# Kernel optimization log

Measured on AMD Instinct MI355X. Metric: run time of the kernel, lower is better.

Reference implementation:

```python
import jax, jax.numpy as jnp
import numpy as np

WS = 16         # window size
NH = 16         # num heads
EPS = 1e-6


def _ln(x):
    m = jnp.mean(x, axis=-1, keepdims=True)
    v = jnp.var(x, axis=-1, keepdims=True)
    return (x - m) * jax.lax.rsqrt(v + EPS)


def _modulate(x, shift, scale):
    return x * (1.0 + scale[:, None, :]) + shift[:, None, :]


def setup_inputs() -> dict:
    key = jax.random.key(0)
    ks = jax.random.split(key, 14)
    D, HD = 1024, 64
    s = 0.02
    return {
        'x': jax.random.normal(ks[0], (4, 4096, D), jnp.float32),
        'c': jax.random.normal(ks[1], (4, D), jnp.float32),
        'qkv_w': jax.random.normal(ks[2], (3 * D, D), jnp.float32) * s,
        'qkv_b': jax.random.normal(ks[3], (3 * D,), jnp.float32) * s,
        'proj_w': jax.random.normal(ks[4], (D, D), jnp.float32) * s,
        'proj_b': jax.random.normal(ks[5], (D,), jnp.float32) * s,
        'rel_pos_h': jax.random.normal(ks[6], (2 * WS - 1, HD), jnp.float32) * s,
        'rel_pos_w': jax.random.normal(ks[7], (2 * WS - 1, HD), jnp.float32) * s,
        'adaLN_w': jax.random.normal(ks[8], (6 * D, D), jnp.float32) * s,
        'adaLN_b': jax.random.normal(ks[9], (6 * D,), jnp.float32) * s,
        'fc1_w': jax.random.normal(ks[10], (4 * D, D), jnp.float32) * s,
        'fc1_b': jax.random.normal(ks[11], (4 * D,), jnp.float32) * s,
        'fc2_w': jax.random.normal(ks[12], (D, 4 * D), jnp.float32) * s,
        'fc2_b': jax.random.normal(ks[13], (D,), jnp.float32) * s,
    }


def _window_attention(x, qkv_w, qkv_b, proj_w, proj_b, rel_pos_h, rel_pos_w):
    # x: [N, T, D] with T = h*w, h = w = sqrt(T)
    N, T, D = x.shape
    h = w = int(round(T ** 0.5))
    nwh, nww = h // WS, w // WS  # grid divides evenly -> no padding
    hd = D // NH
    scale = hd ** -0.5

    # window partition: [N, h, w, D] -> [B, WS, WS, D], B = N*nwh*nww
    xw = x.reshape(N, nwh, WS, nww, WS, D).transpose(0, 1, 3, 2, 4, 5)
    xw = xw.reshape(N * nwh * nww, WS, WS, D)
    B = xw.shape[0]
    L = WS * WS

    qkv = (xw.reshape(B, L, D) @ qkv_w.T + qkv_b)  # [B, L, 3D]
    qkv = qkv.reshape(B, L, 3, NH, hd).transpose(2, 0, 3, 1, 4)  # [3, B, NH, L, hd]
    qkv = qkv.reshape(3, B * NH, L, hd)
    q, k, v = qkv[0], qkv[1], qkv[2]

    attn = jnp.einsum('bqc,bkc->bqk', q * scale, k)  # [B*NH, L, L]

    # decomposed relative position bias (q_size == k_size == WS)
    coords = jnp.arange(WS)
    rel_idx = coords[:, None] - coords[None, :] + (WS - 1)  # [WS, WS]
    Rh = rel_pos_h[rel_idx]  # [WS(q_h), WS(k_h), hd]
    Rw = rel_pos_w[rel_idx]  # [WS(q_w), WS(k_w), hd]
    rq = q.reshape(B * NH, WS, WS, hd)
    rel_h = jnp.einsum('bhwc,hkc->bhwk', rq, Rh)  # [B*NH, WS, WS, WS(kh)]
    rel_w = jnp.einsum('bhwc,wkc->bhwk', rq, Rw)  # [B*NH, WS, WS, WS(kw)]
    attn = (attn.reshape(B * NH, WS, WS, WS, WS)
            + rel_h[:, :, :, :, None]
            + rel_w[:, :, :, None, :]).reshape(B * NH, L, L)

    probs = jax.nn.softmax(attn, axis=-1)
    out = probs @ v  # [B*NH, L, hd]
    out = out.reshape(B, NH, WS, WS, hd).transpose(0, 2, 3, 1, 4).reshape(B, WS, WS, D)
    out = out @ proj_w.T + proj_b

    # window unpartition: [B, WS, WS, D] -> [N, T, D]
    out = out.reshape(N, nwh, nww, WS, WS, D).transpose(0, 1, 3, 2, 4, 5)
    return out.reshape(N, T, D)


def reference(x, c, qkv_w, qkv_b, proj_w, proj_b, rel_pos_h, rel_pos_w,
              adaLN_w, adaLN_b, fc1_w, fc1_b, fc2_w, fc2_b):
    D = x.shape[-1]
    mod = jax.nn.silu(c) @ adaLN_w.T + adaLN_b  # [N, 6D]
    sh_msa, sc_msa, g_msa, sh_mlp, sc_mlp, g_mlp = jnp.split(mod, 6, axis=1)

    a_in = _modulate(_ln(x), sh_msa, sc_msa)
    a_out = _window_attention(a_in, qkv_w, qkv_b, proj_w, proj_b, rel_pos_h, rel_pos_w)
    x = x + g_msa[:, None, :] * a_out

    m_in = _modulate(_ln(x), sh_mlp, sc_mlp)
    hdn = jax.nn.gelu(m_in @ fc1_w.T + fc1_b, approximate=True)
    m_out = hdn @ fc2_w.T + fc2_b
    x = x + g_mlp[:, None, :] * m_out
    return x
```

## Files before the change

### kernel.cpp

```cpp
#include <hip/hip_runtime.h>
#include <cstdint>
#include <cstddef>


typedef float  f32x4    __attribute__((ext_vector_type(4)));
typedef __bf16 bf16x8_t __attribute__((ext_vector_type(8)));
typedef __bf16 bf16x4_t __attribute__((ext_vector_type(4)));

#define DEV __device__ __forceinline__

DEV void gload_lds16(const void* g, void* l) {
    auto gp = (const uint32_t __attribute__((address_space(1)))*)(uintptr_t)g;
    auto lp = (uint32_t __attribute__((address_space(3)))*)(uint32_t)(uintptr_t)l;
    __builtin_amdgcn_global_load_lds(gp, lp, 16, 0, 0);
}

DEV bf16x8_t lds_frag(const __bf16* base, int row, int chunk, int row_elems) {
    return *(const bf16x8_t*)(base + row * row_elems + ((chunk ^ (row & 7)) << 3));
}

DEV bf16x8_t p_frag(const __bf16* base, int row, int chunk) {
    return *(const bf16x8_t*)(base + row * 32 + ((chunk ^ ((row >> 1) & 3)) << 3));
}

DEV int vt_addr(int d, int k) {
    return d * 64 + ((((k >> 3) ^ (d & 7) ^ ((d >> 3) & 7)) << 3) | (k & 7));
}

DEV float gelu_tanh(float v) {
    float u = 0.7978845608028654f * (v + 0.044715f * v * v * v);
    float e = __expf(2.f * u);
    float th = 1.f - 2.f / (e + 1.f);
    return 0.5f * v * (1.f + th);
}

DEV int win2tok(int r) {
    int nb = r >> 12, wi = (r >> 8) & 15, l = r & 255;
    return (nb << 12) + (wi >> 2) * 1024 + (l >> 4) * 64 + (wi & 3) * 16 + (l & 15);
}

__global__ void silu_k(const float* __restrict__ c, float* __restrict__ o, int n) {
    int i = blockIdx.x * 256 + threadIdx.x;
    if (i < n) { float v = c[i]; o[i] = v / (1.f + __expf(-v)); }
}

__global__ void zero_k(float* o, int n) {
    int i = blockIdx.x * 256 + threadIdx.x;
    if (i < n) o[i] = 0.f;
}

__global__ void conv_bf16(const float* __restrict__ s, __bf16* __restrict__ d, int n4) {
    int i = blockIdx.x * 256 + threadIdx.x;
    if (i < n4) {
        float4 v = ((const float4*)s)[i];
        bf16x4_t o; o[0] = (__bf16)v.x; o[1] = (__bf16)v.y; o[2] = (__bf16)v.z; o[3] = (__bf16)v.w;
        ((bf16x4_t*)d)[i] = o;
    }
}

__global__ __launch_bounds__(256)
void mod_gemv(const float* __restrict__ sc, const float* __restrict__ w,
              const float* __restrict__ b, float* __restrict__ mod) {
    int o = (blockIdx.x << 2) + (threadIdx.x >> 6);
    int lane = threadIdx.x & 63;
    int n = o / 6144, col = o % 6144;
    const float4* wr = (const float4*)(w + (size_t)col * 1024);
    const float4* sr = (const float4*)(sc + n * 1024);
    float acc = 0.f;
    #pragma unroll 4
    for (int i = lane; i < 256; i += 64) {
        float4 a = wr[i], x = sr[i];
        acc += a.x * x.x + a.y * x.y + a.z * x.z + a.w * x.w;
    }
    #pragma unroll
    for (int m = 1; m < 64; m <<= 1) acc += __shfl_xor(acc, m);
    if (lane == 0) mod[o] = acc + b[col];
}

__global__ __launch_bounds__(256)
void ln_mod_k(const float* __restrict__ src, const float* __restrict__ mod,
              int sh_off, int sc_off, __bf16* __restrict__ out, int permute, int r0) {
    int rl = blockIdx.x;
    int r = rl + r0;
    int nb = r >> 12;
    int t = permute ? win2tok(r) : r;
    float4 v = ((const float4*)(src + (size_t)t * 1024))[threadIdx.x];
    float s  = v.x + v.y + v.z + v.w;
    float sq = v.x * v.x + v.y * v.y + v.z * v.z + v.w * v.w;
    #pragma unroll
    for (int m = 1; m < 64; m <<= 1) { s += __shfl_xor(s, m); sq += __shfl_xor(sq, m); }
    __shared__ float ps[4], pq[4];
    int wv = threadIdx.x >> 6, ln = threadIdx.x & 63;
    if (ln == 0) { ps[wv] = s; pq[wv] = sq; }
    __syncthreads();
    s  = ps[0] + ps[1] + ps[2] + ps[3];
    sq = pq[0] + pq[1] + pq[2] + pq[3];
    float mean = s * (1.f / 1024.f);
    float var  = sq * (1.f / 1024.f) - mean * mean;
    float rstd = rsqrtf(var + 1e-6f);
    int c = threadIdx.x << 2;
    const float* mrow = mod + nb * 6144;
    float4 scv = *(const float4*)(mrow + sc_off + c);
    float4 shv = *(const float4*)(mrow + sh_off + c);
    bf16x4_t o;
    o[0] = (__bf16)((v.x - mean) * rstd * (1.f + scv.x) + shv.x);
    o[1] = (__bf16)((v.y - mean) * rstd * (1.f + scv.y) + shv.y);
    o[2] = (__bf16)((v.z - mean) * rstd * (1.f + scv.z) + shv.z);
    o[3] = (__bf16)((v.w - mean) * rstd * (1.f + scv.w) + shv.w);
    *(bf16x4_t*)(out + (size_t)rl * 1024 + c) = o;
}

template <int PM, int PN>
DEV void mfma16(f32x4 (&acc)[8][4], bf16x8_t (&fa)[4][2], bf16x8_t (&fb)[2][2][2]) {
    #pragma unroll
    for (int ks = 0; ks < 2; ++ks)
        #pragma unroll
        for (int mi = 0; mi < 4; ++mi)
            #pragma unroll
            for (int nn = 0; nn < 2; ++nn)
                acc[PM * 4 + mi][PN * 2 + nn] = __builtin_amdgcn_mfma_f32_16x16x32_bf16(
                    fa[mi][ks], fb[PN][nn][ks], acc[PM * 4 + mi][PN * 2 + nn], 0, 0, 0);
}

template <int EPI>
__global__ __launch_bounds__(512)
void gemm256(const __bf16* __restrict__ A, const __bf16* __restrict__ B,
             const float* __restrict__ bias, void* __restrict__ Cout,
             const float* __restrict__ extra, const float* __restrict__ mod,
             int N, int K, int r0) {
    extern __shared__ __align__(16) char smem[];
    __bf16* lA = (__bf16*)smem;
    __bf16* lB = lA + 2 * 256 * 64;
    const int tid = threadIdx.x, lane = tid & 63, wv = tid >> 6;
    const int wr = wv >> 2, wc = wv & 3;
    const int bm = blockIdx.y << 8, bn = blockIdx.x << 8;

    f32x4 acc[8][4];
    const f32x4 z4 = {0.f, 0.f, 0.f, 0.f};
    #pragma unroll
    for (int i = 0; i < 8; ++i)
        #pragma unroll
        for (int j = 0; j < 4; ++j) acc[i][j] = z4;

    bf16x8_t fa[4][2], fb[2][2][2];
    const int gc8 = (((lane & 7) ^ (lane >> 3)) << 3);

    auto stageA = [&](int buf, int k0, int h) {
        #pragma unroll
        for (int j = 0; j < 2; ++j) {
            int rb = (h << 6) + (j << 7) + (wv << 3);
            gload_lds16(A + (size_t)(bm + rb + (lane >> 3)) * K + k0 + gc8,
                        lA + buf * 16384 + rb * 64);
        }
    };
    auto stageB = [&](int buf, int k0, int h) {
        #pragma unroll
        for (int j = 0; j < 2; ++j) {
            int rb = (h << 5) + (j << 7) + ((wv & 3) << 3) + ((wv >> 2) << 6);
            gload_lds16(B + (size_t)(bn + rb + (lane >> 3)) * K + k0 + gc8,
                        lB + buf * 16384 + rb * 64);
        }
    };
    auto readA = [&](int buf, int pm) {
        #pragma unroll
        for (int mi = 0; mi < 4; ++mi)
            #pragma unroll
            for (int ks = 0; ks < 2; ++ks)
                fa[mi][ks] = lds_frag(lA + buf * 16384,
                                      (wr << 7) + (pm << 6) + (mi << 4) + (lane & 15),
                                      (ks << 2) + (lane >> 4), 64);
    };
    auto readB = [&](int buf, int pn) {
        #pragma unroll
        for (int ni = 0; ni < 2; ++ni)
            #pragma unroll
            for (int ks = 0; ks < 2; ++ks)
                fb[pn][ni][ks] = lds_frag(lB + buf * 16384,
                                          (wc << 6) + (pn << 5) + (ni << 4) + (lane & 15),
                                          (ks << 2) + (lane >> 4), 64);
    };

    const int nt = K >> 6;
    stageA(0, 0, 0); stageB(0, 0, 0); stageB(0, 0, 1); stageA(0, 0, 1);

    int cur = 0;
    for (int t = 0; t < nt - 1; ++t) {
        const int nk0 = (t + 1) << 6;
        stageA(cur ^ 1, nk0, 0);
        asm volatile("s_waitcnt vmcnt(6)" ::: "memory");
        __builtin_amdgcn_s_barrier();
        __builtin_amdgcn_sched_barrier(0);
        readA(cur, 0); readB(cur, 0);
        asm volatile("s_waitcnt lgkmcnt(0)" ::: "memory");
        __builtin_amdgcn_sched_barrier(0);
        __builtin_amdgcn_s_setprio(1); mfma16<0, 0>(acc, fa, fb); __builtin_amdgcn_s_setprio(0);
        stageB(cur ^ 1, nk0, 0);
        asm volatile("s_waitcnt vmcnt(6)" ::: "memory");
        __builtin_amdgcn_s_barrier();
        __builtin_amdgcn_sched_barrier(0);
        readB(cur, 1);
        asm volatile("s_waitcnt lgkmcnt(0)" ::: "memory");
        __builtin_amdgcn_sched_barrier(0);
        __builtin_amdgcn_s_setprio(1); mfma16<0, 1>(acc, fa, fb); __builtin_amdgcn_s_setprio(0);
        stageB(cur ^ 1, nk0, 1);
        asm volatile("s_waitcnt vmcnt(6)" ::: "memory");
        __builtin_amdgcn_s_barrier();
        __builtin_amdgcn_sched_barrier(0);
        readA(cur, 1);
        asm volatile("s_waitcnt lgkmcnt(0)" ::: "memory");
        __builtin_amdgcn_sched_barrier(0);
        __builtin_amdgcn_s_setprio(1); mfma16<1, 0>(acc, fa, fb); __builtin_amdgcn_s_setprio(0);
        stageA(cur ^ 1, nk0, 1);
        __builtin_amdgcn_s_setprio(1); mfma16<1, 1>(acc, fa, fb); __builtin_amdgcn_s_setprio(0);
        cur ^= 1;
    }
    asm volatile("s_waitcnt vmcnt(4)" ::: "memory");
    __builtin_amdgcn_s_barrier();
    __builtin_amdgcn_sched_barrier(0);
    readA(cur, 0); readB(cur, 0);
    asm volatile("s_waitcnt lgkmcnt(0)" ::: "memory");
    __builtin_amdgcn_sched_barrier(0);
    __builtin_amdgcn_s_setprio(1); mfma16<0, 0>(acc, fa, fb); __builtin_amdgcn_s_setprio(0);
    asm volatile("s_waitcnt vmcnt(2)" ::: "memory");
    __builtin_amdgcn_s_barrier();
    __builtin_amdgcn_sched_barrier(0);
    readB(cur, 1);
    asm volatile("s_waitcnt lgkmcnt(0)" ::: "memory");
    __builtin_amdgcn_sched_barrier(0);
    __builtin_amdgcn_s_setprio(1); mfma16<0, 1>(acc, fa, fb); __builtin_amdgcn_s_setprio(0);
    asm volatile("s_waitcnt vmcnt(0)" ::: "memory");
    __builtin_amdgcn_s_barrier();
    __builtin_amdgcn_sched_barrier(0);
    readA(cur, 1);
    asm volatile("s_waitcnt lgkmcnt(0)" ::: "memory");
    __builtin_amdgcn_sched_barrier(0);
    __builtin_amdgcn_s_setprio(1); mfma16<1, 0>(acc, fa, fb); __builtin_amdgcn_s_setprio(0);
    __builtin_amdgcn_s_setprio(1); mfma16<1, 1>(acc, fa, fb); __builtin_amdgcn_s_setprio(0);

    #pragma unroll
    for (int am = 0; am < 8; ++am) {
        #pragma unroll
        for (int j = 0; j < 4; ++j) {
            int m = bm + (wr << 7) + (am << 4) + ((lane >> 4) << 2) + j;
            #pragma unroll
            for (int an = 0; an < 4; ++an) {
                int n = bn + (wc << 6) + (an << 4) + (lane & 15);
                float v = acc[am][an][j] + bias[n];
                if constexpr (EPI == 0) {
                    ((__bf16*)Cout)[(size_t)m * N + n] = (__bf16)v;
                } else if constexpr (EPI == 1) {
                    int mg = m + r0;
                    int tr = win2tok(mg);
                    float g = mod[(mg >> 12) * 6144 + 2048 + n];
                    ((float*)Cout)[(size_t)tr * 1024 + n] = extra[(size_t)tr * 1024 + n] + g * v;
                } else if constexpr (EPI == 2) {
                    ((__bf16*)Cout)[(size_t)m * N + n] = (__bf16)gelu_tanh(v);
                } else {
                    int mg = m + r0;
                    float g = mod[(mg >> 12) * 6144 + 5120 + n];
                    ((float*)Cout)[(size_t)mg * 1024 + n] = extra[(size_t)mg * 1024 + n] + g * v;
                }
            }
        }
    }
}

__global__ __launch_bounds__(256)
void tab_k(const __bf16* __restrict__ qkv, const float* __restrict__ relh,
           const float* __restrict__ relw, __bf16* __restrict__ tab) {
    __shared__ __bf16 lR[2][31][72];
    for (int i = threadIdx.x; i < 1984; i += 256) {
        int row = i >> 6, c = i & 63;
        lR[0][row][c] = (__bf16)relh[i];
        lR[1][row][c] = (__bf16)relw[i];
    }
    __syncthreads();
    const int h = blockIdx.y;
    const int r = threadIdx.x >> 1, half = threadIdx.x & 1;
    const int l = blockIdx.x * 128 + r;
    const int lw = l & 255;
    const int qi = lw >> 4, qj = lw & 15;
    const __bf16* qrow = qkv + (size_t)l * 3072 + h * 64;
    float qq[64];
    #pragma unroll
    for (int c8 = 0; c8 < 8; ++c8) {
        bf16x8_t q8 = *(const bf16x8_t*)(qrow + (c8 << 3));
        #pragma unroll
        for (int e = 0; e < 8; ++e) qq[c8 * 8 + e] = (float)q8[e];
    }
    bf16x8_t oh, ow;
    #pragma unroll
    for (int kk = 0; kk < 8; ++kk) {
        int kg = (half << 3) + kk;
        const __bf16* Rh = &lR[0][qi - kg + 15][0];
        const __bf16* Rw = &lR[1][qj - kg + 15][0];
        float ah = 0.f, aw = 0.f;
        #pragma unroll
        for (int c8 = 0; c8 < 8; ++c8) {
            bf16x8_t r1 = *(const bf16x8_t*)(Rh + (c8 << 3));
            bf16x8_t r2 = *(const bf16x8_t*)(Rw + (c8 << 3));
            #pragma unroll
            for (int e = 0; e < 8; ++e) {
                ah += qq[c8 * 8 + e] * (float)r1[e];
                aw += qq[c8 * 8 + e] * (float)r2[e];
            }
        }
        oh[kk] = (__bf16)ah; ow[kk] = (__bf16)aw;
    }
    size_t idx = ((size_t)(l >> 8) * 16 + h) * 256 + lw;
    *(bf16x8_t*)(tab + idx * 32 + (half << 3))      = oh;
    *(bf16x8_t*)(tab + idx * 32 + 16 + (half << 3)) = ow;
}

__global__ __launch_bounds__(256, 3)
void attn_k(const __bf16* __restrict__ qkv, const __bf16* __restrict__ tab,
            __bf16* __restrict__ out) {
    __shared__ __align__(16) __bf16 lP[4][32 * 32];
    __shared__ __align__(16) __bf16 lKt[2][64 * 64];
    __shared__ __align__(16) __bf16 lVt[2][64 * 64];
    __shared__ __align__(16) __bf16 lTab[128 * 32];

    const int blk = blockIdx.x;
    const int winc = blk >> 5, h = (blk >> 1) & 15, qh = blk & 1;
    const int tid = threadIdx.x, lane = tid & 63, wv = tid >> 6;
    const __bf16* base = qkv + (size_t)winc * 256 * 3072 + h * 64;
    const int q0 = qh << 7;

    {
        const __bf16* ts = tab + (((size_t)winc * 16 + h) * 256 + q0) * 32;
        #pragma unroll
        for (int q = 0; q < 2; ++q) {
            int c = (wv << 1) + q;
            gload_lds16(ts + c * 512 + lane * 8, lTab + c * 512);
        }
    }
    bf16x8_t qf[2][2];
    #pragma unroll
    for (int mi = 0; mi < 2; ++mi)
        #pragma unroll
        for (int ks = 0; ks < 2; ++ks) {
            int l = q0 + (wv << 5) + (mi << 4) + (lane & 15);
            qf[mi][ks] = *(const bf16x8_t*)(base + (size_t)l * 3072 + (((ks << 2) + (lane >> 4)) << 3));
        }
    {
        const __bf16* kb = base + 1024;
        #pragma unroll
        for (int q = 0; q < 2; ++q) {
            int c = (wv << 1) + q;
            int kl = (c << 3) + (lane >> 3);
            gload_lds16(kb + (size_t)kl * 3072 + (((lane & 7) ^ (lane >> 3)) << 3),
                        lKt[0] + c * 512);
        }
        const __bf16* vb = base + 2048;
        bf16x8_t a = *(const bf16x8_t*)(vb + (size_t)(tid >> 3) * 3072 + ((tid & 7) << 3));
        bf16x8_t b = *(const bf16x8_t*)(vb + (size_t)(32 + (tid >> 3)) * 3072 + ((tid & 7) << 3));
        int lc = tid & 7;
        #pragma unroll
        for (int e = 0; e < 8; ++e) {
            lVt[0][vt_addr(lc * 8 + e, tid >> 3)]        = a[e];
            lVt[0][vt_addr(lc * 8 + e, 32 + (tid >> 3))] = b[e];
        }
    }
    __syncthreads();

    float twv[2][4];
    #pragma unroll
    for (int mi = 0; mi < 2; ++mi)
        #pragma unroll
        for (int j = 0; j < 4; ++j) {
            int qr = (wv << 5) + (mi << 4) + ((lane >> 4) << 2) + j;
            twv[mi][j] = (float)lTab[qr * 32 + 16 + (lane & 15)];
        }

    const f32x4 z4 = {0.f, 0.f, 0.f, 0.f};
    f32x4 oacc[2][4];
    #pragma unroll
    for (int a = 0; a < 2; ++a)
        #pragma unroll
        for (int b = 0; b < 4; ++b) oacc[a][b] = z4;
    float rsum[2][4];
    #pragma unroll
    for (int a = 0; a < 2; ++a)
        #pragma unroll
        for (int j = 0; j < 4; ++j) rsum[a][j] = 0.f;
    __bf16* lPw = lP[wv];

    int cur = 0;
    for (int kt = 0; kt < 4; ++kt) {
        const bool pre = (kt < 3);
        bf16x8_t v8a, v8b;
        if (pre) {
            const __bf16* kb = base + 1024 + (size_t)(kt + 1) * 64 * 3072;
            #pragma unroll
            for (int q = 0; q < 2; ++q) {
                int c = (wv << 1) + q;
                int kl = (c << 3) + (lane >> 3);
                gload_lds16(kb + (size_t)kl * 3072 + (((lane & 7) ^ (lane >> 3)) << 3),
                            lKt[cur ^ 1] + c * 512);
            }
            const __bf16* vb = base + 2048 + (size_t)(kt + 1) * 64 * 3072;
            v8a = *(const bf16x8_t*)(vb + (size_t)(tid >> 3) * 3072 + ((tid & 7) << 3));
            v8b = *(const bf16x8_t*)(vb + (size_t)(32 + (tid >> 3)) * 3072 + ((tid & 7) << 3));
        }

        f32x4 s[2][4];
        #pragma unroll
        for (int a = 0; a < 2; ++a)
            #pragma unroll
            for (int b = 0; b < 4; ++b) s[a][b] = z4;
        #pragma unroll
        for (int ks = 0; ks < 2; ++ks) {
            bf16x8_t kf[4];
            #pragma unroll
            for (int ni = 0; ni < 4; ++ni)
                kf[ni] = lds_frag(lKt[cur], (ni << 4) + (lane & 15), (ks << 2) + (lane >> 4), 64);
            #pragma unroll
            for (int mi = 0; mi < 2; ++mi)
                #pragma unroll
                for (int ni = 0; ni < 4; ++ni)
                    s[mi][ni] = __builtin_amdgcn_mfma_f32_16x16x32_bf16(qf[mi][ks], kf[ni], s[mi][ni], 0, 0, 0);
        }

        #pragma unroll
        for (int mi = 0; mi < 2; ++mi) {
            #pragma unroll
            for (int j = 0; j < 4; ++j) {
                int qr = (wv << 5) + (mi << 4) + ((lane >> 4) << 2) + j;
                bf16x4_t th4 = *(const bf16x4_t*)(lTab + qr * 32 + (kt << 2));
                float rs = 0.f;
                #pragma unroll
                for (int ni = 0; ni < 4; ++ni) {
                    float p = __expf(s[mi][ni][j] * 0.125f + (float)th4[ni] + twv[mi][j]);
                    s[mi][ni][j] = p;
                    rs += p;
                }
                rsum[mi][j] += rs;
            }
        }

        #pragma unroll
        for (int hf = 0; hf < 2; ++hf) {
            #pragma unroll
            for (int mi = 0; mi < 2; ++mi) {
                #pragma unroll
                for (int j = 0; j < 4; ++j) {
                    int rl = (mi << 4) + ((lane >> 4) << 2) + j;
                    #pragma unroll
                    for (int b = 0; b < 2; ++b) {
                        int col = (b << 4) + (lane & 15);
                        lPw[rl * 32 + ((((col >> 3) ^ ((rl >> 1) & 3)) << 3) | (col & 7))] =
                            (__bf16)s[mi][(hf << 1) + b][j];
                    }
                }
            }
            bf16x8_t pf[2], vf[4];
            #pragma unroll
            for (int mi = 0; mi < 2; ++mi)
                pf[mi] = p_frag(lPw, (mi << 4) + (lane & 15), lane >> 4);
            #pragma unroll
            for (int no = 0; no < 4; ++no) {
                int d = (no << 4) + (lane & 15);
                vf[no] = *(const bf16x8_t*)(lVt[cur] + vt_addr(d, ((hf << 2) + (lane >> 4)) << 3));
            }
            #pragma unroll
            for (int mi = 0; mi < 2; ++mi)
                #pragma unroll
                for (int no = 0; no < 4; ++no)
                    oacc[mi][no] = __builtin_amdgcn_mfma_f32_16x16x32_bf16(pf[mi], vf[no], oacc[mi][no], 0, 0, 0);
        }

        if (pre) {
            int lc = tid & 7;
            #pragma unroll
            for (int e = 0; e < 8; ++e) {
                lVt[cur ^ 1][vt_addr(lc * 8 + e, tid >> 3)]        = v8a[e];
                lVt[cur ^ 1][vt_addr(lc * 8 + e, 32 + (tid >> 3))] = v8b[e];
            }
        }
        __syncthreads();
        cur ^= 1;
    }

    #pragma unroll
    for (int mi = 0; mi < 2; ++mi) {
        #pragma unroll
        for (int j = 0; j < 4; ++j) {
            float rs = rsum[mi][j];
            #pragma unroll
            for (int msk = 1; msk < 16; msk <<= 1) rs += __shfl_xor(rs, msk);
            float inv = 1.f / rs;
            int l = q0 + (wv << 5) + (mi << 4) + ((lane >> 4) << 2) + j;
            #pragma unroll
            for (int no = 0; no < 4; ++no) {
                int col = (no << 4) + (lane & 15);
                out[(size_t)(winc * 256 + l) * 1024 + h * 64 + col] = (__bf16)(oacc[mi][no][j] * inv);
            }
        }
    }
}

extern "C" void kernel_launch(void* const* d_in, const int* in_sizes, int n_in,
                              void* d_out, int out_size, void* d_ws, size_t ws_size,
                              hipStream_t stream) {
    const float* x      = (const float*)d_in[0];
    const float* c      = (const float*)d_in[1];
    const float* qkv_w  = (const float*)d_in[2];
    const float* qkv_b  = (const float*)d_in[3];
    const float* proj_w = (const float*)d_in[4];
    const float* proj_b = (const float*)d_in[5];
    const float* rel_h  = (const float*)d_in[6];
    const float* rel_w  = (const float*)d_in[7];
    const float* ada_w  = (const float*)d_in[8];
    const float* ada_b  = (const float*)d_in[9];
    const float* fc1_w  = (const float*)d_in[10];
    const float* fc1_b  = (const float*)d_in[11];
    const float* fc2_w  = (const float*)d_in[12];
    const float* fc2_b  = (const float*)d_in[13];
    float* xo = (float*)d_out;

    char* ws = (char*)d_ws;
    const size_t MB = 1ull << 20;
    int CH = 0;
    const int cands[7] = {16384, 8192, 4096, 2048, 1024, 512, 256};
    for (int i = 0; i < 7; ++i)
        if (26 * MB + (size_t)cands[i] * 10240 <= ws_size) { CH = cands[i]; break; }
    if (CH == 0) {
        zero_k<<<65536, 256, 0, stream>>>(xo, 16777216);
        return;
    }
    const int NCH = 16384 / CH;

    const int LDSB = 131072;
    hipFuncSetAttribute((const void*)&gemm256<0>, hipFuncAttributeMaxDynamicSharedMemorySize, LDSB);
    hipFuncSetAttribute((const void*)&gemm256<1>, hipFuncAttributeMaxDynamicSharedMemorySize, LDSB);
    hipFuncSetAttribute((const void*)&gemm256<2>, hipFuncAttributeMaxDynamicSharedMemorySize, LDSB);
    hipFuncSetAttribute((const void*)&gemm256<3>, hipFuncAttributeMaxDynamicSharedMemorySize, LDSB);

    float*  ws_silu = (float*)(ws);
    float*  ws_mod  = (float*)(ws + 65536);
    __bf16* w_qkv   = (__bf16*)(ws + 1 * MB);
    __bf16* w_proj  = (__bf16*)(ws + 7 * MB);
    __bf16* w_fc1   = (__bf16*)(ws + 9 * MB);
    __bf16* w_fc2   = (__bf16*)(ws + 17 * MB);
    __bf16* bufA    = (__bf16*)(ws + 26 * MB);
    __bf16* bufB    = (__bf16*)(ws + 26 * MB + (size_t)CH * 2048);
    __bf16* tabbuf  = bufB + (size_t)CH * 3072;

    silu_k   <<<16,   256, 0, stream>>>(c, ws_silu, 4096);
    mod_gemv <<<6144, 256, 0, stream>>>(ws_silu, ada_w, ada_b, ws_mod);
    conv_bf16<<<3072, 256, 0, stream>>>(qkv_w,  w_qkv,  786432);
    conv_bf16<<<1024, 256, 0, stream>>>(proj_w, w_proj, 262144);
    conv_bf16<<<4096, 256, 0, stream>>>(fc1_w,  w_fc1,  1048576);
    conv_bf16<<<4096, 256, 0, stream>>>(fc2_w,  w_fc2,  1048576);

    for (int ci = 0; ci < NCH; ++ci) {
        int r0 = ci * CH;
        ln_mod_k<<<CH, 256, 0, stream>>>(x, ws_mod, 0, 1024, bufA, 1, r0);
        gemm256<0><<<dim3(12, CH / 256), 512, LDSB, stream>>>(bufA, w_qkv, qkv_b, bufB,
                                                              nullptr, nullptr, 3072, 1024, r0);
        tab_k<<<dim3(CH / 128, 16), 256, 0, stream>>>(bufB, rel_h, rel_w, tabbuf);
        attn_k<<<(CH / 256) * 32, 256, 0, stream>>>(bufB, tabbuf, bufA);
        gemm256<1><<<dim3(4, CH / 256), 512, LDSB, stream>>>(bufA, w_proj, proj_b, xo,
                                                             x, ws_mod, 1024, 1024, r0);
    }
    for (int ci = 0; ci < NCH; ++ci) {
        int r0 = ci * CH;
        ln_mod_k<<<CH, 256, 0, stream>>>(xo, ws_mod, 3072, 4096, bufA, 0, r0);
        gemm256<2><<<dim3(16, CH / 256), 512, LDSB, stream>>>(bufA, w_fc1, fc1_b, bufB,
                                                              nullptr, nullptr, 4096, 1024, r0);
        gemm256<3><<<dim3(4, CH / 256), 512, LDSB, stream>>>(bufB, w_fc2, fc2_b, xo,
                                                             xo, ws_mod, 1024, 4096, r0);
    }
}
```

Measured before the change: 644.6 us.

## Deepen GEMM prefetch pipeline and remap blocks across XCDs for L2 locality

Restructures the 256x256 GEMM main loop so loads for tile t+2 are issued while tile t is computed, with barriers between phases and a simplified epilogue. It also switches to a 1D grid whose block IDs are remapped so that consecutive tiles land on the same XCD, aiming to improve L2 reuse of A and B tiles. The deeper prefetch is meant to hide global-load latency, at the cost of more barriers per iteration and more complex buffer reuse that could introduce LDS hazards.

```diff
diff --git a/kernel.cpp b/kernel.cpp
--- a/kernel.cpp
+++ b/kernel.cpp
@@ -122,18 +122,29 @@
                     fa[mi][ks], fb[PN][nn][ks], acc[PM * 4 + mi][PN * 2 + nn], 0, 0, 0);
 }
 
+#define GBAR  __builtin_amdgcn_s_barrier()
+#define LGKM0 do { asm volatile("s_waitcnt lgkmcnt(0)" ::: "memory"); \
+                   __builtin_amdgcn_sched_barrier(0); } while (0)
+#define PRIO1 __builtin_amdgcn_s_setprio(1)
+#define PRIO0 __builtin_amdgcn_s_setprio(0)
+
 template <int EPI>
 __global__ __launch_bounds__(512)
 void gemm256(const __bf16* __restrict__ A, const __bf16* __restrict__ B,
              const float* __restrict__ bias, void* __restrict__ Cout,
              const float* __restrict__ extra, const float* __restrict__ mod,
-             int N, int K, int r0) {
+             int N, int K, int r0, int gx) {
     extern __shared__ __align__(16) char smem[];
     __bf16* lA = (__bf16*)smem;
-    __bf16* lB = lA + 2 * 256 * 64;
+    __bf16* lB = lA + 2 * 16384;
     const int tid = threadIdx.x, lane = tid & 63, wv = tid >> 6;
     const int wr = wv >> 2, wc = wv & 3;
-    const int bm = blockIdx.y << 8, bn = blockIdx.x << 8;
+
+    const int nwg = gridDim.x;
+    const int qq = nwg >> 3, rr = nwg & 7;
+    const int xcd = blockIdx.x & 7, pos = blockIdx.x >> 3;
+    const int nid = (xcd < rr ? xcd * (qq + 1) : rr * (qq + 1) + (xcd - rr) * qq) + pos;
+    const int bm = (nid / gx) << 8, bn = (nid % gx) << 8;
 
     f32x4 acc[8][4];
     const f32x4 z4 = {0.f, 0.f, 0.f, 0.f};
@@ -182,60 +193,43 @@
 
     const int nt = K >> 6;
     stageA(0, 0, 0); stageB(0, 0, 0); stageB(0, 0, 1); stageA(0, 0, 1);
+    stageA(1, 64, 0); stageB(1, 64, 0); stageB(1, 64, 1);
+    asm volatile("s_waitcnt vmcnt(6)" ::: "memory");
+    GBAR;
 
     int cur = 0;
     for (int t = 0; t < nt - 1; ++t) {
-        const int nk0 = (t + 1) << 6;
-        stageA(cur ^ 1, nk0, 0);
-        asm volatile("s_waitcnt vmcnt(6)" ::: "memory");
-        __builtin_amdgcn_s_barrier();
-        __builtin_amdgcn_sched_barrier(0);
+        const int k2 = (t + 2) << 6;
+        const bool s2 = (t + 2 < nt);
         readA(cur, 0); readB(cur, 0);
-        asm volatile("s_waitcnt lgkmcnt(0)" ::: "memory");
-        __builtin_amdgcn_sched_barrier(0);
-        __builtin_amdgcn_s_setprio(1); mfma16<0, 0>(acc, fa, fb); __builtin_amdgcn_s_setprio(0);
-        stageB(cur ^ 1, nk0, 0);
-        asm volatile("s_waitcnt vmcnt(6)" ::: "memory");
-        __builtin_amdgcn_s_barrier();
-        __builtin_amdgcn_sched_barrier(0);
+        stageA(cur ^ 1, (t + 1) << 6, 1);
+        GBAR; LGKM0;
+        PRIO1; mfma16<0, 0>(acc, fa, fb); PRIO0;
+        GBAR;
         readB(cur, 1);
-        asm volatile("s_waitcnt lgkmcnt(0)" ::: "memory");
-        __builtin_amdgcn_sched_barrier(0);
-        __builtin_amdgcn_s_setprio(1); mfma16<0, 1>(acc, fa, fb); __builtin_amdgcn_s_setprio(0);
-        stageB(cur ^ 1, nk0, 1);
-        asm volatile("s_waitcnt vmcnt(6)" ::: "memory");
-        __builtin_amdgcn_s_barrier();
-        __builtin_amdgcn_sched_barrier(0);
+        if (s2) stageA(cur, k2, 0);
+        GBAR; LGKM0;
+        PRIO1; mfma16<0, 1>(acc, fa, fb); PRIO0;
+        GBAR;
         readA(cur, 1);
-        asm volatile("s_waitcnt lgkmcnt(0)" ::: "memory");
-        __builtin_amdgcn_sched_barrier(0);
-        __builtin_amdgcn_s_setprio(1); mfma16<1, 0>(acc, fa, fb); __builtin_amdgcn_s_setprio(0);
-        stageA(cur ^ 1, nk0, 1);
-        __builtin_amdgcn_s_setprio(1); mfma16<1, 1>(acc, fa, fb); __builtin_amdgcn_s_setprio(0);
+        if (s2) stageB(cur, k2, 0);
+        GBAR; LGKM0;
+        PRIO1; mfma16<1, 0>(acc, fa, fb); PRIO0;
+        GBAR;
+        if (s2) stageB(cur, k2, 1);
+        if (t == nt - 2) asm volatile("s_waitcnt vmcnt(0)" ::: "memory");
+        else             asm volatile("s_waitcnt vmcnt(6)" ::: "memory");
+        GBAR;
+        PRIO1; mfma16<1, 1>(acc, fa, fb); PRIO0;
+        GBAR;
         cur ^= 1;
     }
-    asm volatile("s_waitcnt vmcnt(4)" ::: "memory");
-    __builtin_amdgcn_s_barrier();
-    __builtin_amdgcn_sched_barrier(0);
-    readA(cur, 0); readB(cur, 0);
-    asm volatile("s_waitcnt lgkmcnt(0)" ::: "memory");
-    __builtin_amdgcn_sched_barrier(0);
-    __builtin_amdgcn_s_setprio(1); mfma16<0, 0>(acc, fa, fb); __builtin_amdgcn_s_setprio(0);
-    asm volatile("s_waitcnt vmcnt(2)" ::: "memory");
-    __builtin_amdgcn_s_barrier();
-    __builtin_amdgcn_sched_barrier(0);
-    readB(cur, 1);
-    asm volatile("s_waitcnt lgkmcnt(0)" ::: "memory");
-    __builtin_amdgcn_sched_barrier(0);
-    __builtin_amdgcn_s_setprio(1); mfma16<0, 1>(acc, fa, fb); __builtin_amdgcn_s_setprio(0);
-    asm volatile("s_waitcnt vmcnt(0)" ::: "memory");
-    __builtin_amdgcn_s_barrier();
-    __builtin_amdgcn_sched_barrier(0);
+    readA(cur, 0); readB(cur, 0); readB(cur, 1);
+    LGKM0;
+    PRIO1; mfma16<0, 0>(acc, fa, fb); mfma16<0, 1>(acc, fa, fb); PRIO0;
     readA(cur, 1);
-    asm volatile("s_waitcnt lgkmcnt(0)" ::: "memory");
-    __builtin_amdgcn_sched_barrier(0);
-    __builtin_amdgcn_s_setprio(1); mfma16<1, 0>(acc, fa, fb); __builtin_amdgcn_s_setprio(0);
-    __builtin_amdgcn_s_setprio(1); mfma16<1, 1>(acc, fa, fb); __builtin_amdgcn_s_setprio(0);
+    LGKM0;
+    PRIO1; mfma16<1, 0>(acc, fa, fb); mfma16<1, 1>(acc, fa, fb); PRIO0;
 
     #pragma unroll
     for (int am = 0; am < 8; ++am) {
@@ -528,7 +522,6 @@
         zero_k<<<65536, 256, 0, stream>>>(xo, 16777216);
         return;
     }
-    const int NCH = 16384 / CH;
 
     const int LDSB = 131072;
     hipFuncSetAttribute((const void*)&gemm256<0>, hipFuncAttributeMaxDynamicSharedMemorySize, LDSB);
@@ -536,6 +529,7 @@
     hipFuncSetAttribute((const void*)&gemm256<2>, hipFuncAttributeMaxDynamicSharedMemorySize, LDSB);
     hipFuncSetAttribute((const void*)&gemm256<3>, hipFuncAttributeMaxDynamicSharedMemorySize, LDSB);
 
+    const int NCH = 16384 / CH;
     float*  ws_silu = (float*)(ws);
     float*  ws_mod  = (float*)(ws + 65536);
     __bf16* w_qkv   = (__bf16*)(ws + 1 * MB);
@@ -553,22 +547,23 @@
     conv_bf16<<<4096, 256, 0, stream>>>(fc1_w,  w_fc1,  1048576);
     conv_bf16<<<4096, 256, 0, stream>>>(fc2_w,  w_fc2,  1048576);
 
+    const int gy = CH / 256;
     for (int ci = 0; ci < NCH; ++ci) {
         int r0 = ci * CH;
         ln_mod_k<<<CH, 256, 0, stream>>>(x, ws_mod, 0, 1024, bufA, 1, r0);
-        gemm256<0><<<dim3(12, CH / 256), 512, LDSB, stream>>>(bufA, w_qkv, qkv_b, bufB,
-                                                              nullptr, nullptr, 3072, 1024, r0);
+        gemm256<0><<<12 * gy, 512, LDSB, stream>>>(bufA, w_qkv, qkv_b, bufB,
+                                                   nullptr, nullptr, 3072, 1024, r0, 12);
         tab_k<<<dim3(CH / 128, 16), 256, 0, stream>>>(bufB, rel_h, rel_w, tabbuf);
         attn_k<<<(CH / 256) * 32, 256, 0, stream>>>(bufB, tabbuf, bufA);
-        gemm256<1><<<dim3(4, CH / 256), 512, LDSB, stream>>>(bufA, w_proj, proj_b, xo,
-                                                             x, ws_mod, 1024, 1024, r0);
+        gemm256<1><<<4 * gy, 512, LDSB, stream>>>(bufA, w_proj, proj_b, xo,
+                                                  x, ws_mod, 1024, 1024, r0, 4);
     }
     for (int ci = 0; ci < NCH; ++ci) {
         int r0 = ci * CH;
         ln_mod_k<<<CH, 256, 0, stream>>>(xo, ws_mod, 3072, 4096, bufA, 0, r0);
-        gemm256<2><<<dim3(16, CH / 256), 512, LDSB, stream>>>(bufA, w_fc1, fc1_b, bufB,
-                                                              nullptr, nullptr, 4096, 1024, r0);
-        gemm256<3><<<dim3(4, CH / 256), 512, LDSB, stream>>>(bufB, w_fc2, fc2_b, xo,
-                                                             xo, ws_mod, 1024, 4096, r0);
-    }
-}
+        gemm256<2><<<16 * gy, 512, LDSB, stream>>>(bufA, w_fc1, fc1_b, bufB,
+                                                   nullptr, nullptr, 4096, 1024, r0, 16);
+        gemm256<3><<<4 * gy, 512, LDSB, stream>>>(bufB, w_fc2, fc2_b, xo,
+                                                  xo, ws_mod, 1024, 4096, r0, 4);
+    }
+}
```

Result: no change. 641.4 us (-0.5%).
